# Performance work log

Hardware: AMD Instinct MI355X
Metric: run time of the kernel (lower is better)

## Reference

```python
import jax, jax.numpy as jnp
import numpy as np

N_NODES = 50000
N_EDGES = 800000
D_IN, D_HID, D_OUT = 128, 128, 64


def _gcn_conv(x, row, col, W, b, num_nodes):
    # Linear (no bias in lin; bias added after aggregation)
    h = x @ W  # [N, d_out]
    # degree over destination (col), includes self-loops
    deg = jax.ops.segment_sum(jnp.ones_like(col, dtype=h.dtype), col, num_segments=num_nodes)
    dis = jnp.where(deg > 0, deg ** -0.5, 0.0)  # deg^{-1/2}, inf -> 0
    norm = dis[row] * dis[col]  # [E+N]
    msg = h[row] * norm[:, None]  # gather + scale
    out = jax.ops.segment_sum(msg, col, num_segments=num_nodes)  # scatter-add
    return out + b


def setup_inputs() -> dict:
    key = jax.random.key(0)
    k1, k2, k3, k4 = jax.random.split(key, 4)
    x = jax.random.normal(k1, (N_NODES, D_IN), dtype=jnp.float32)
    edge_index = jax.random.randint(k2, (2, N_EDGES), 0, N_NODES, dtype=jnp.int32)
    # glorot-like init for linear weights
    W1 = jax.random.normal(k3, (D_IN, D_HID), dtype=jnp.float32) * (2.0 / (D_IN + D_HID)) ** 0.5
    W2 = jax.random.normal(k4, (D_HID, D_OUT), dtype=jnp.float32) * (2.0 / (D_HID + D_OUT)) ** 0.5
    b1 = jnp.zeros((D_HID,), dtype=jnp.float32)
    b2 = jnp.zeros((D_OUT,), dtype=jnp.float32)
    return {"x": x, "edge_index": edge_index, "W1": W1, "b1": b1, "W2": W2, "b2": b2}


def reference(x, edge_index, W1, b1, W2, b2):
    n = x.shape[0]
    # add self-loops
    loops = jnp.arange(n, dtype=edge_index.dtype)
    row = jnp.concatenate([edge_index[0], loops])
    col = jnp.concatenate([edge_index[1], loops])
    h = _gcn_conv(x, row, col, W1, b1, n)
    h = jax.nn.relu(h)  # dropout is identity in eval mode
    out = _gcn_conv(h, row, col, W2, b2, n)
    return out
```

## Files before the change

kernel.cpp:

```cpp
#include <hip/hip_runtime.h>

#define BSH 7
#define BMSK 127
#define NB 391
#define ROWSH 13
#define RCH 7
#define SEG (NB * RCH)
#define NBLK 128
#define BINCAP 3072

typedef __attribute__((ext_vector_type(8))) short short8;
typedef __attribute__((ext_vector_type(4))) float f32x4;
typedef __attribute__((ext_vector_type(4))) unsigned int u32x4;

static inline size_t alignup(size_t x) { return (x + 255) & ~(size_t)255; }

__device__ __forceinline__ unsigned short f2bf(float f) {
    unsigned int u = __float_as_uint(f);
    u = (u + 0x7fffu + ((u >> 16) & 1u)) >> 16;
    return (unsigned short)u;
}

__global__ __launch_bounds__(256) void k_hist(const int* __restrict__ colp,
                                              const int* __restrict__ rowp, int nE,
                                              unsigned* __restrict__ counts,
                                              const float* __restrict__ W1,
                                              const float* __restrict__ W2,
                                              unsigned short* __restrict__ Wt1,
                                              unsigned short* __restrict__ Wt2) {
    int blk = blockIdx.x;
    if (blk >= NBLK) {
        int i = (blk - NBLK) * 256 + threadIdx.x;
        if (i < 128 * 128) { int k = i >> 7, c = i & 127; Wt1[(size_t)c * 128 + k] = f2bf(W1[i]); }
        if (i < 128 * 64)  { int k = i >> 6, c = i & 63;  Wt2[(size_t)c * 128 + k] = f2bf(W2[i]); }
        return;
    }
    __shared__ unsigned h[SEG];
    for (int i = threadIdx.x; i < SEG; i += 256) h[i] = 0;
    __syncthreads();
    int chunk = (nE + NBLK - 1) / NBLK;
    int e0 = blk * chunk, e1 = min(nE, e0 + chunk);
    for (int e = e0 + (int)threadIdx.x; e < e1; e += 256) {
        int c = colp[e], r = rowp[e];
        atomicAdd(&h[(c >> BSH) * RCH + (r >> ROWSH)], 1u);
    }
    __syncthreads();
    for (int i = threadIdx.x; i < SEG; i += 256) counts[(size_t)i * NBLK + blk] = h[i];
}

__global__ __launch_bounds__(128) void k_scanA(unsigned* __restrict__ counts,
                                               unsigned* __restrict__ segtot) {
    int seg = blockIdx.x, t = threadIdx.x;
    __shared__ unsigned ps[NBLK];
    unsigned s = counts[(size_t)seg * NBLK + t];
    ps[t] = s;
    __syncthreads();
    for (int d = 1; d < NBLK; d <<= 1) {
        unsigned v = (t >= d) ? ps[t - d] : 0u;
        __syncthreads();
        ps[t] += v;
        __syncthreads();
    }
    counts[(size_t)seg * NBLK + t] = ps[t] - s;
    if (t == NBLK - 1) segtot[seg] = ps[NBLK - 1];
}

__global__ __launch_bounds__(256) void k_scanB(const unsigned* __restrict__ segtot,
                                               unsigned* __restrict__ segbase,
                                               unsigned* __restrict__ edgebase, int nE) {
    __shared__ unsigned ls[SEG];
    __shared__ unsigned ts[256];
    int t = threadIdx.x;
    for (int i = t; i < SEG; i += 256) ls[i] = segtot[i];
    __syncthreads();
    const int CH = (SEG + 255) / 256;
    unsigned s = 0;
#pragma unroll
    for (int j = 0; j < CH; ++j) {
        int idx = t * CH + j;
        if (idx < SEG) s += ls[idx];
    }
    ts[t] = s;
    __syncthreads();
    for (int d = 1; d < 256; d <<= 1) {
        unsigned v = (t >= d) ? ts[t - d] : 0u;
        __syncthreads();
        ts[t] += v;
        __syncthreads();
    }
    unsigned run = ts[t] - s;
    unsigned loc[CH > 0 ? CH : 1];
#pragma unroll
    for (int j = 0; j < CH; ++j) {
        int idx = t * CH + j;
        if (idx < SEG) { unsigned v = ls[idx]; loc[j] = run; segbase[idx] = run; run += v; }
    }
    __syncthreads();
#pragma unroll
    for (int j = 0; j < CH; ++j) {
        int idx = t * CH + j;
        if (idx < SEG) ls[idx] = loc[j];
    }
    __syncthreads();
    for (int b = t; b < NB; b += 256) edgebase[b] = ls[b * RCH];
    if (t == 0) edgebase[NB] = (unsigned)nE;
}

__global__ __launch_bounds__(256) void k_scatter(const int* __restrict__ colp,
                                                 const int* __restrict__ rowp, int nE,
                                                 const unsigned* __restrict__ counts,
                                                 const unsigned* __restrict__ segbase,
                                                 unsigned* __restrict__ pairs) {
    __shared__ unsigned cur[SEG];
    int blk = blockIdx.x;
    for (int i = threadIdx.x; i < SEG; i += 256)
        cur[i] = segbase[i] + counts[(size_t)i * NBLK + blk];
    __syncthreads();
    int chunk = (nE + NBLK - 1) / NBLK;
    int e0 = blk * chunk, e1 = min(nE, e0 + chunk);
    for (int e = e0 + (int)threadIdx.x; e < e1; e += 256) {
        int c = colp[e], r = rowp[e];
        unsigned pos = atomicAdd(&cur[(c >> BSH) * RCH + (r >> ROWSH)], 1u);
        pairs[pos] = ((unsigned)r << BSH) | (unsigned)(c & BMSK);
    }
}

__global__ __launch_bounds__(256) void k_binbuild(const unsigned* __restrict__ pairs,
                                                  const unsigned* __restrict__ edgebase,
                                                  unsigned* __restrict__ csr,
                                                  unsigned* __restrict__ off,
                                                  float* __restrict__ dis, int n) {
    __shared__ unsigned lp[BINCAP];
    __shared__ unsigned lr[BINCAP];
    __shared__ unsigned hist[128];
    __shared__ unsigned scn[128];
    int b = blockIdx.x, t = threadIdx.x;
    unsigned e0 = edgebase[b], e1 = edgebase[b + 1];
    unsigned ec = e1 - e0;
    if (ec > BINCAP) ec = BINCAP;
    if (t < 128) hist[t] = 0;
    __syncthreads();
    for (unsigned i = t; i < ec; i += 256) {
        unsigned v = pairs[e0 + i];
        lp[i] = v;
        atomicAdd(&hist[v & BMSK], 1u);
    }
    __syncthreads();
    unsigned hv = (t < 128) ? hist[t] : 0u;
    if (t < 128) scn[t] = hv;
    __syncthreads();
    for (int d = 1; d < 128; d <<= 1) {
        unsigned v = (t < 128 && t >= d) ? scn[t - d] : 0u;
        __syncthreads();
        if (t < 128) scn[t] += v;
        __syncthreads();
    }
    unsigned ex = (t < 128) ? scn[t] - hv : 0u;
    int node = (b << BSH) + t;
    if (t < 128 && node < n) {
        off[node] = e0 + ex;
        dis[node] = rsqrtf((float)(hv + 1));
    }
    if (b == NB - 1 && t == 0) off[n] = e1;
    __syncthreads();
    if (t < 128) scn[t] = ex;
    __syncthreads();
    for (unsigned i = t; i < ec; i += 256) {
        unsigned v = lp[i];
        unsigned pos = atomicAdd(&scn[v & BMSK], 1u);
        lr[pos] = v >> BSH;
    }
    __syncthreads();
    for (unsigned i = t; i < ec; i += 256) csr[e0 + i] = lr[i];
}

__global__ __launch_bounds__(256) void k_gemm1(const float* __restrict__ x,
                                               const unsigned short* __restrict__ Wt1,
                                               const float* __restrict__ dis,
                                               unsigned short* __restrict__ hs1, int M) {
    const int NT = 8;
    const int lane = threadIdx.x & 63;
    const int wave = threadIdx.x >> 6;
    const int m0 = blockIdx.x * 64 + wave * 16;
    const int lrow = lane & 15;
    const int lk = lane >> 4;
    int arow = m0 + lrow;
    if (arow >= M) arow = M - 1;

    f32x4 acc[NT];
#pragma unroll
    for (int t = 0; t < NT; ++t) acc[t] = (f32x4){0.f, 0.f, 0.f, 0.f};

#pragma unroll
    for (int k0 = 0; k0 < 4; ++k0) {
        const int kb = k0 * 32 + lk * 8;
        const float* ap = &x[(size_t)arow * 128 + kb];
        f32x4 v0 = __builtin_nontemporal_load((const f32x4*)ap);
        f32x4 v1 = __builtin_nontemporal_load((const f32x4*)(ap + 4));
        short8 afrag;
#pragma unroll
        for (int q = 0; q < 4; ++q) {
            afrag[q] = (short)f2bf(v0[q]);
            afrag[4 + q] = (short)f2bf(v1[q]);
        }
#pragma unroll
        for (int t = 0; t < NT; ++t) {
            const int bcol = t * 16 + lrow;
            short8 bfrag = *(const short8*)&Wt1[(size_t)bcol * 128 + kb];
            acc[t] = __builtin_amdgcn_mfma_f32_16x16x32_bf16(afrag, bfrag, acc[t], 0, 0, 0);
        }
    }

#pragma unroll
    for (int i = 0; i < 4; ++i) {
        int row = m0 + lk * 4 + i;
        if (row < M) {
            float s = dis[row];
#pragma unroll
            for (int t = 0; t < NT; ++t)
                hs1[(size_t)row * 128 + t * 16 + lrow] = f2bf(acc[t][i] * s);
        }
    }
}

__device__ __forceinline__ void acc8(float a[8], u32x4 u) {
    a[0] += __uint_as_float(u[0] << 16);
    a[1] += __uint_as_float(u[0] & 0xffff0000u);
    a[2] += __uint_as_float(u[1] << 16);
    a[3] += __uint_as_float(u[1] & 0xffff0000u);
    a[4] += __uint_as_float(u[2] << 16);
    a[5] += __uint_as_float(u[2] & 0xffff0000u);
    a[6] += __uint_as_float(u[3] << 16);
    a[7] += __uint_as_float(u[3] & 0xffff0000u);
}

__global__ __launch_bounds__(256) void k_fuse2(const unsigned short* __restrict__ hs1,
                                               const unsigned* __restrict__ csr,
                                               const unsigned* __restrict__ off,
                                               const float* __restrict__ dis,
                                               const float* __restrict__ b1,
                                               const unsigned short* __restrict__ Wt2,
                                               unsigned short* __restrict__ hs2, int n) {
    __shared__ unsigned short st[16 * 136];
    const int tid = threadIdx.x;
    int vloc = tid >> 4;
    int c = tid & 15;
    int v = blockIdx.x * 16 + vloc;
    if (v >= n) v = n - 1;

    const u32x4* h4 = (const u32x4*)hs1;
    size_t base = (size_t)v * 16 + c;
    unsigned s = off[v], e = off[v + 1];
    float dv = dis[v];

    float a[8];
#pragma unroll
    for (int j = 0; j < 8; ++j) a[j] = 0.f;
    acc8(a, h4[base]);

    unsigned i = s;
    for (; i + 4 <= e; i += 4) {
        unsigned r0 = csr[i], r1 = csr[i + 1], r2 = csr[i + 2], r3 = csr[i + 3];
        u32x4 m0 = h4[(size_t)r0 * 16 + c];
        u32x4 m1 = h4[(size_t)r1 * 16 + c];
        u32x4 m2 = h4[(size_t)r2 * 16 + c];
        u32x4 m3 = h4[(size_t)r3 * 16 + c];
        acc8(a, m0); acc8(a, m1); acc8(a, m2); acc8(a, m3);
    }
    for (; i < e; ++i) acc8(a, h4[(size_t)csr[i] * 16 + c]);

    u32x4 pk;
#pragma unroll
    for (int q = 0; q < 4; ++q) {
        float lo = fmaxf(a[2 * q] * dv + b1[c * 8 + 2 * q], 0.f);
        float hi = fmaxf(a[2 * q + 1] * dv + b1[c * 8 + 2 * q + 1], 0.f);
        pk[q] = (unsigned)f2bf(lo) | ((unsigned)f2bf(hi) << 16);
    }
    *(u32x4*)&st[vloc * 136 + c * 8] = pk;
    __syncthreads();

    const int lane = tid & 63;
    const int wave = tid >> 6;
    const int lrow = lane & 15;
    const int lk = lane >> 4;
    f32x4 acc = (f32x4){0.f, 0.f, 0.f, 0.f};
#pragma unroll
    for (int k0 = 0; k0 < 4; ++k0) {
        const int kb = k0 * 32 + lk * 8;
        short8 afrag = *(const short8*)&st[lrow * 136 + kb];
        const int bcol = wave * 16 + lrow;
        short8 bfrag = *(const short8*)&Wt2[(size_t)bcol * 128 + kb];
        acc = __builtin_amdgcn_mfma_f32_16x16x32_bf16(afrag, bfrag, acc, 0, 0, 0);
    }
#pragma unroll
    for (int i2 = 0; i2 < 4; ++i2) {
        int row = blockIdx.x * 16 + lk * 4 + i2;
        if (row < n) {
            float sc = dis[row];
            hs2[(size_t)row * 64 + wave * 16 + lrow] = f2bf(acc[i2] * sc);
        }
    }
}

__global__ __launch_bounds__(256) void k_gather2(const unsigned short* __restrict__ hs,
                                                 const unsigned* __restrict__ csr,
                                                 const unsigned* __restrict__ off,
                                                 const float* __restrict__ dis,
                                                 const float* __restrict__ bias,
                                                 float* __restrict__ outp, int n) {
    int v = blockIdx.x * 32 + (int)(threadIdx.x >> 3);
    int c = threadIdx.x & 7;
    if (v >= n) return;
    const u32x4* h4 = (const u32x4*)hs;
    size_t base = (size_t)v * 8 + c;

    unsigned s = off[v], e = off[v + 1];
    float dv = dis[v];

    float a[8];
#pragma unroll
    for (int j = 0; j < 8; ++j) a[j] = 0.f;
    acc8(a, h4[base]);

    unsigned i = s;
    for (; i + 4 <= e; i += 4) {
        unsigned r0 = csr[i], r1 = csr[i + 1], r2 = csr[i + 2], r3 = csr[i + 3];
        u32x4 m0 = h4[(size_t)r0 * 8 + c];
        u32x4 m1 = h4[(size_t)r1 * 8 + c];
        u32x4 m2 = h4[(size_t)r2 * 8 + c];
        u32x4 m3 = h4[(size_t)r3 * 8 + c];
        acc8(a, m0); acc8(a, m1); acc8(a, m2); acc8(a, m3);
    }
    for (; i < e; ++i) acc8(a, h4[(size_t)csr[i] * 8 + c]);

    float rr[8];
#pragma unroll
    for (int j = 0; j < 8; ++j) rr[j] = a[j] * dv + bias[c * 8 + j];
    f32x4 lov = {rr[0], rr[1], rr[2], rr[3]};
    f32x4 hiv = {rr[4], rr[5], rr[6], rr[7]};
    __builtin_nontemporal_store(lov, (f32x4*)&outp[(size_t)v * 64 + c * 8]);
    __builtin_nontemporal_store(hiv, (f32x4*)&outp[(size_t)v * 64 + c * 8 + 4]);
}

extern "C" void kernel_launch(void* const* d_in, const int* in_sizes, int n_in,
                              void* d_out, int out_size, void* d_ws, size_t ws_size,
                              hipStream_t stream) {
    const float* x  = (const float*)d_in[0];
    const int*   ei = (const int*)d_in[1];
    const float* W1 = (const float*)d_in[2];
    const float* b1 = (const float*)d_in[3];
    const float* W2 = (const float*)d_in[4];
    const float* b2 = (const float*)d_in[5];

    const int Din = 128;
    const int Nn = in_sizes[0] / Din;
    const int E  = in_sizes[1] / 2;
    const int* rowp = ei;
    const int* colp = ei + E;

    char* ws = (char*)d_ws;
    size_t off_ = 0;
    unsigned*       counts   = (unsigned*)(ws + off_);       off_ = alignup(off_ + (size_t)SEG * NBLK * 4);
    unsigned*       segtot   = (unsigned*)(ws + off_);       off_ = alignup(off_ + (size_t)SEG * 4);
    unsigned*       segbase  = (unsigned*)(ws + off_);       off_ = alignup(off_ + (size_t)SEG * 4);
    unsigned*       edgebase = (unsigned*)(ws + off_);       off_ = alignup(off_ + (size_t)(NB + 1) * 4);
    unsigned*       pairs    = (unsigned*)(ws + off_);       off_ = alignup(off_ + (size_t)E * 4);
    unsigned*       csr      = (unsigned*)(ws + off_);       off_ = alignup(off_ + (size_t)E * 4);
    unsigned*       offv     = (unsigned*)(ws + off_);       off_ = alignup(off_ + (size_t)(Nn + 1) * 4);
    float*          dis      = (float*)(ws + off_);          off_ = alignup(off_ + (size_t)Nn * 4);
    unsigned short* Wt1      = (unsigned short*)(ws + off_); off_ = alignup(off_ + 128 * 128 * 2);
    unsigned short* Wt2      = (unsigned short*)(ws + off_); off_ = alignup(off_ + 128 * 64 * 2);
    unsigned short* hs1      = (unsigned short*)(ws + off_); off_ = alignup(off_ + (size_t)Nn * 128 * 2);
    unsigned short* hs2      = (unsigned short*)(ws + off_); off_ = alignup(off_ + (size_t)Nn * 64 * 2);
    float*          outp     = (float*)d_out;

    k_hist<<<NBLK + 64, 256, 0, stream>>>(colp, rowp, E, counts, W1, W2, Wt1, Wt2);
    k_scanA<<<SEG, NBLK, 0, stream>>>(counts, segtot);
    k_scanB<<<1, 256, 0, stream>>>(segtot, segbase, edgebase, E);
    k_scatter<<<NBLK, 256, 0, stream>>>(colp, rowp, E, counts, segbase, pairs);
    k_binbuild<<<NB, 256, 0, stream>>>(pairs, edgebase, csr, offv, dis, Nn);

    k_gemm1<<<(Nn + 63) / 64, 256, 0, stream>>>(x, Wt1, dis, hs1, Nn);

    k_fuse2<<<(Nn + 15) / 16, 256, 0, stream>>>(hs1, csr, offv, dis, b1, Wt2, hs2, Nn);

    k_gather2<<<(Nn + 31) / 32, 256, 0, stream>>>(hs2, csr, offv, dis, b2, outp, Nn);
}
```

Baseline: 122.1 us.

## Overlap layer-1 GEMM with edge histogram and merge scan kernels

Moves the dis scaling out of the first GEMM so that GEMM no longer depends on the CSR build. It can then run in the same launch as the edge histogram, with different blocks doing different work. The two scan kernels are merged into one using a last-block-done atomic counter, and NBLK is doubled to 256. In exchange, fuse2 now gathers dis[r] for every edge and applies it per neighbour, which adds irregular loads and FMAs to the aggregation loop. The extra k_prep launch also resets the done counter.

New measurement: 290.8 us. 2.38x slower.

```diff
diff --git a/kernel.cpp b/kernel.cpp
--- a/kernel.cpp
+++ b/kernel.cpp
@@ -6,7 +6,7 @@
 #define ROWSH 13
 #define RCH 7
 #define SEG (NB * RCH)
-#define NBLK 128
+#define NBLK 256
 #define BINCAP 3072
 
 typedef __attribute__((ext_vector_type(8))) short short8;
@@ -21,56 +21,110 @@
     return (unsigned short)u;
 }
 
-__global__ __launch_bounds__(256) void k_hist(const int* __restrict__ colp,
-                                              const int* __restrict__ rowp, int nE,
-                                              unsigned* __restrict__ counts,
-                                              const float* __restrict__ W1,
+__global__ __launch_bounds__(256) void k_prep(const float* __restrict__ W1,
                                               const float* __restrict__ W2,
                                               unsigned short* __restrict__ Wt1,
-                                              unsigned short* __restrict__ Wt2) {
-    int blk = blockIdx.x;
-    if (blk >= NBLK) {
-        int i = (blk - NBLK) * 256 + threadIdx.x;
-        if (i < 128 * 128) { int k = i >> 7, c = i & 127; Wt1[(size_t)c * 128 + k] = f2bf(W1[i]); }
-        if (i < 128 * 64)  { int k = i >> 6, c = i & 63;  Wt2[(size_t)c * 128 + k] = f2bf(W2[i]); }
+                                              unsigned short* __restrict__ Wt2,
+                                              unsigned* __restrict__ done) {
+    int i = blockIdx.x * 256 + threadIdx.x;
+    if (i == 0) *done = 0u;
+    if (i < 128 * 128) { int k = i >> 7, c = i & 127; Wt1[(size_t)c * 128 + k] = f2bf(W1[i]); }
+    if (i < 128 * 64)  { int k = i >> 6, c = i & 63;  Wt2[(size_t)c * 128 + k] = f2bf(W2[i]); }
+}
+
+__global__ __launch_bounds__(256) void k_front(const float* __restrict__ x,
+                                               const unsigned short* __restrict__ Wt1,
+                                               unsigned short* __restrict__ hs1, int M,
+                                               const int* __restrict__ colp,
+                                               const int* __restrict__ rowp, int nE,
+                                               unsigned* __restrict__ counts, int G1) {
+    if ((int)blockIdx.x >= G1) {
+        int blk = blockIdx.x - G1;
+        __shared__ unsigned h[SEG];
+        for (int i = threadIdx.x; i < SEG; i += 256) h[i] = 0;
+        __syncthreads();
+        int chunk = (nE + NBLK - 1) / NBLK;
+        int e0 = blk * chunk, e1 = min(nE, e0 + chunk);
+        for (int e = e0 + (int)threadIdx.x; e < e1; e += 256) {
+            int c = colp[e], r = rowp[e];
+            atomicAdd(&h[(c >> BSH) * RCH + (r >> ROWSH)], 1u);
+        }
+        __syncthreads();
+        for (int i = threadIdx.x; i < SEG; i += 256) counts[(size_t)i * NBLK + blk] = h[i];
         return;
     }
-    __shared__ unsigned h[SEG];
-    for (int i = threadIdx.x; i < SEG; i += 256) h[i] = 0;
-    __syncthreads();
-    int chunk = (nE + NBLK - 1) / NBLK;
-    int e0 = blk * chunk, e1 = min(nE, e0 + chunk);
-    for (int e = e0 + (int)threadIdx.x; e < e1; e += 256) {
-        int c = colp[e], r = rowp[e];
-        atomicAdd(&h[(c >> BSH) * RCH + (r >> ROWSH)], 1u);
-    }
-    __syncthreads();
-    for (int i = threadIdx.x; i < SEG; i += 256) counts[(size_t)i * NBLK + blk] = h[i];
-}
-
-__global__ __launch_bounds__(128) void k_scanA(unsigned* __restrict__ counts,
-                                               unsigned* __restrict__ segtot) {
+    const int NT = 8;
+    const int lane = threadIdx.x & 63;
+    const int wave = threadIdx.x >> 6;
+    const int m0 = blockIdx.x * 64 + wave * 16;
+    const int lrow = lane & 15;
+    const int lk = lane >> 4;
+    int arow = m0 + lrow;
+    if (arow >= M) arow = M - 1;
+
+    f32x4 acc[NT];
+#pragma unroll
+    for (int t = 0; t < NT; ++t) acc[t] = (f32x4){0.f, 0.f, 0.f, 0.f};
+
+#pragma unroll
+    for (int k0 = 0; k0 < 4; ++k0) {
+        const int kb = k0 * 32 + lk * 8;
+        const float* ap = &x[(size_t)arow * 128 + kb];
+        f32x4 v0 = __builtin_nontemporal_load((const f32x4*)ap);
+        f32x4 v1 = __builtin_nontemporal_load((const f32x4*)(ap + 4));
+        short8 afrag;
+#pragma unroll
+        for (int q = 0; q < 4; ++q) {
+            afrag[q] = (short)f2bf(v0[q]);
+            afrag[4 + q] = (short)f2bf(v1[q]);
+        }
+#pragma unroll
+        for (int t = 0; t < NT; ++t) {
+            const int bcol = t * 16 + lrow;
+            short8 bfrag = *(const short8*)&Wt1[(size_t)bcol * 128 + kb];
+            acc[t] = __builtin_amdgcn_mfma_f32_16x16x32_bf16(afrag, bfrag, acc[t], 0, 0, 0);
+        }
+    }
+#pragma unroll
+    for (int i = 0; i < 4; ++i) {
+        int row = m0 + lk * 4 + i;
+        if (row < M) {
+#pragma unroll
+            for (int t = 0; t < NT; ++t)
+                hs1[(size_t)row * 128 + t * 16 + lrow] = f2bf(acc[t][i]);
+        }
+    }
+}
+
+__global__ __launch_bounds__(256) void k_scanAB(unsigned* __restrict__ counts,
+                                                unsigned* __restrict__ segtot,
+                                                unsigned* __restrict__ segbase,
+                                                unsigned* __restrict__ edgebase, int nE,
+                                                unsigned* __restrict__ done) {
     int seg = blockIdx.x, t = threadIdx.x;
-    __shared__ unsigned ps[NBLK];
-    unsigned s = counts[(size_t)seg * NBLK + t];
-    ps[t] = s;
-    __syncthreads();
-    for (int d = 1; d < NBLK; d <<= 1) {
-        unsigned v = (t >= d) ? ps[t - d] : 0u;
-        __syncthreads();
-        ps[t] += v;
-        __syncthreads();
-    }
-    counts[(size_t)seg * NBLK + t] = ps[t] - s;
-    if (t == NBLK - 1) segtot[seg] = ps[NBLK - 1];
-}
-
-__global__ __launch_bounds__(256) void k_scanB(const unsigned* __restrict__ segtot,
-                                               unsigned* __restrict__ segbase,
-                                               unsigned* __restrict__ edgebase, int nE) {
+    {
+        __shared__ unsigned ps[NBLK];
+        unsigned s = counts[(size_t)seg * NBLK + t];
+        ps[t] = s;
+        __syncthreads();
+        for (int d = 1; d < NBLK; d <<= 1) {
+            unsigned v = (t >= d) ? ps[t - d] : 0u;
+            __syncthreads();
+            ps[t] += v;
+            __syncthreads();
+        }
+        counts[(size_t)seg * NBLK + t] = ps[t] - s;
+        if (t == NBLK - 1) segtot[seg] = ps[NBLK - 1];
+    }
+    __threadfence();
+    __shared__ bool lastf;
+    if (t == 0) lastf = (atomicAdd(done, 1u) == SEG - 1);
+    __syncthreads();
+    if (!lastf) return;
+    __threadfence();
+
     __shared__ unsigned ls[SEG];
     __shared__ unsigned ts[256];
-    int t = threadIdx.x;
     for (int i = t; i < SEG; i += 256) ls[i] = segtot[i];
     __syncthreads();
     const int CH = (SEG + 255) / 256;
@@ -174,53 +228,15 @@
     for (unsigned i = t; i < ec; i += 256) csr[e0 + i] = lr[i];
 }
 
-__global__ __launch_bounds__(256) void k_gemm1(const float* __restrict__ x,
-                                               const unsigned short* __restrict__ Wt1,
-                                               const float* __restrict__ dis,
-                                               unsigned short* __restrict__ hs1, int M) {
-    const int NT = 8;
-    const int lane = threadIdx.x & 63;
-    const int wave = threadIdx.x >> 6;
-    const int m0 = blockIdx.x * 64 + wave * 16;
-    const int lrow = lane & 15;
-    const int lk = lane >> 4;
-    int arow = m0 + lrow;
-    if (arow >= M) arow = M - 1;
-
-    f32x4 acc[NT];
-#pragma unroll
-    for (int t = 0; t < NT; ++t) acc[t] = (f32x4){0.f, 0.f, 0.f, 0.f};
-
-#pragma unroll
-    for (int k0 = 0; k0 < 4; ++k0) {
-        const int kb = k0 * 32 + lk * 8;
-        const float* ap = &x[(size_t)arow * 128 + kb];
-        f32x4 v0 = __builtin_nontemporal_load((const f32x4*)ap);
-        f32x4 v1 = __builtin_nontemporal_load((const f32x4*)(ap + 4));
-        short8 afrag;
-#pragma unroll
-        for (int q = 0; q < 4; ++q) {
-            afrag[q] = (short)f2bf(v0[q]);
-            afrag[4 + q] = (short)f2bf(v1[q]);
-        }
-#pragma unroll
-        for (int t = 0; t < NT; ++t) {
-            const int bcol = t * 16 + lrow;
-            short8 bfrag = *(const short8*)&Wt1[(size_t)bcol * 128 + kb];
-            acc[t] = __builtin_amdgcn_mfma_f32_16x16x32_bf16(afrag, bfrag, acc[t], 0, 0, 0);
-        }
-    }
-
-#pragma unroll
-    for (int i = 0; i < 4; ++i) {
-        int row = m0 + lk * 4 + i;
-        if (row < M) {
-            float s = dis[row];
-#pragma unroll
-            for (int t = 0; t < NT; ++t)
-                hs1[(size_t)row * 128 + t * 16 + lrow] = f2bf(acc[t][i] * s);
-        }
-    }
+__device__ __forceinline__ void acc8s(float a[8], u32x4 u, float d) {
+    a[0] = fmaf(__uint_as_float(u[0] << 16), d, a[0]);
+    a[1] = fmaf(__uint_as_float(u[0] & 0xffff0000u), d, a[1]);
+    a[2] = fmaf(__uint_as_float(u[1] << 16), d, a[2]);
+    a[3] = fmaf(__uint_as_float(u[1] & 0xffff0000u), d, a[3]);
+    a[4] = fmaf(__uint_as_float(u[2] << 16), d, a[4]);
+    a[5] = fmaf(__uint_as_float(u[2] & 0xffff0000u), d, a[5]);
+    a[6] = fmaf(__uint_as_float(u[3] << 16), d, a[6]);
+    a[7] = fmaf(__uint_as_float(u[3] & 0xffff0000u), d, a[7]);
 }
 
 __device__ __forceinline__ void acc8(float a[8], u32x4 u) {
@@ -256,18 +272,22 @@
     float a[8];
 #pragma unroll
     for (int j = 0; j < 8; ++j) a[j] = 0.f;
-    acc8(a, h4[base]);
+    acc8s(a, h4[base], dv);
 
     unsigned i = s;
     for (; i + 4 <= e; i += 4) {
         unsigned r0 = csr[i], r1 = csr[i + 1], r2 = csr[i + 2], r3 = csr[i + 3];
+        float d0 = dis[r0], d1 = dis[r1], d2 = dis[r2], d3 = dis[r3];
         u32x4 m0 = h4[(size_t)r0 * 16 + c];
         u32x4 m1 = h4[(size_t)r1 * 16 + c];
         u32x4 m2 = h4[(size_t)r2 * 16 + c];
         u32x4 m3 = h4[(size_t)r3 * 16 + c];
-        acc8(a, m0); acc8(a, m1); acc8(a, m2); acc8(a, m3);
-    }
-    for (; i < e; ++i) acc8(a, h4[(size_t)csr[i] * 16 + c]);
+        acc8s(a, m0, d0); acc8s(a, m1, d1); acc8s(a, m2, d2); acc8s(a, m3, d3);
+    }
+    for (; i < e; ++i) {
+        unsigned r = csr[i];
+        acc8s(a, h4[(size_t)r * 16 + c], dis[r]);
+    }
 
     u32x4 pk;
 #pragma unroll
@@ -364,6 +384,7 @@
     unsigned*       segtot   = (unsigned*)(ws + off_);       off_ = alignup(off_ + (size_t)SEG * 4);
     unsigned*       segbase  = (unsigned*)(ws + off_);       off_ = alignup(off_ + (size_t)SEG * 4);
     unsigned*       edgebase = (unsigned*)(ws + off_);       off_ = alignup(off_ + (size_t)(NB + 1) * 4);
+    unsigned*       done     = (unsigned*)(ws + off_);       off_ = alignup(off_ + 256);
     unsigned*       pairs    = (unsigned*)(ws + off_);       off_ = alignup(off_ + (size_t)E * 4);
     unsigned*       csr      = (unsigned*)(ws + off_);       off_ = alignup(off_ + (size_t)E * 4);
     unsigned*       offv     = (unsigned*)(ws + off_);       off_ = alignup(off_ + (size_t)(Nn + 1) * 4);
@@ -374,14 +395,17 @@
     unsigned short* hs2      = (unsigned short*)(ws + off_); off_ = alignup(off_ + (size_t)Nn * 64 * 2);
     float*          outp     = (float*)d_out;
 
-    k_hist<<<NBLK + 64, 256, 0, stream>>>(colp, rowp, E, counts, W1, W2, Wt1, Wt2);
-    k_scanA<<<SEG, NBLK, 0, stream>>>(counts, segtot);
-    k_scanB<<<1, 256, 0, stream>>>(segtot, segbase, edgebase, E);
+    const int G1 = (Nn + 63) / 64;
+
+    k_prep<<<64, 256, 0, stream>>>(W1, W2, Wt1, Wt2, done);
+
+    k_front<<<G1 + NBLK, 256, 0, stream>>>(x, Wt1, hs1, Nn, colp, rowp, E, counts, G1);
+
+    k_scanAB<<<SEG, NBLK, 0, stream>>>(counts, segtot, segbase, edgebase, E, done);
+
     k_scatter<<<NBLK, 256, 0, stream>>>(colp, rowp, E, counts, segbase, pairs);
     k_binbuild<<<NB, 256, 0, stream>>>(pairs, edgebase, csr, offv, dis, Nn);
 
-    k_gemm1<<<(Nn + 63) / 64, 256, 0, stream>>>(x, Wt1, dis, hs1, Nn);
-
     k_fuse2<<<(Nn + 15) / 16, 256, 0, stream>>>(hs1, csr, offv, dis, b1, Wt2, hs2, Nn);
 
     k_gather2<<<(Nn + 31) / 32, 256, 0, stream>>>(hs2, csr, offv, dis, b2, outp, Nn);
```
